# Kernel optimization log

Hardware: AMD Instinct MI355X
Metric: run time of the kernel (lower is better)

## Reference

```python
import jax, jax.numpy as jnp
import numpy as np

SAMPLING_FACTOR = 5


def setup_inputs() -> dict:
    key = jax.random.key(0)
    kq, kk, kv, ki = jax.random.split(key, 4)
    B, L, D = 32, 2048, 64
    return {
        "query_states": jax.random.normal(kq, (B, L, D), dtype=jnp.float32),
        "key_states": jax.random.normal(kk, (B, L, D), dtype=jnp.float32),
        "value_states": jax.random.normal(kv, (B, L, D), dtype=jnp.float32),
        "index_sample": jax.random.randint(ki, (L,), 0, L, dtype=jnp.int32),
    }


def reference(query_states, key_states, value_states, index_sample):
    B, L_Q, d_k = query_states.shape
    L_K = key_states.shape[1]
    log_L_K = int(np.ceil(np.log1p(L_K)))
    log_L_Q = int(np.ceil(np.log1p(L_Q)))
    U_part = min(SAMPLING_FACTOR * L_Q * log_L_K, L_K)
    u = min(SAMPLING_FACTOR * log_L_Q, L_Q)

    # random key sampling (indices supplied deterministically)
    idx = index_sample[:U_part]                       # [U_part]
    K_sample = jnp.take(key_states, idx, axis=1)      # [B, U_part, d]

    # sparsity measurement M(q) = max_k q.k - mean (original divides by L_K)
    Q_K_sample = jnp.einsum("bqd,bkd->bqk", query_states, K_sample)  # [B, L_Q, U_part]
    M = jnp.max(Q_K_sample, axis=-1) - jnp.sum(Q_K_sample, axis=-1) / jnp.float32(L_K)

    # top-u query selection
    _, M_top = jax.lax.top_k(M, u)                    # [B, u]
    Q_reduce = jnp.take_along_axis(query_states, M_top[..., None], axis=1)  # [B, u, d]

    # reduced attention
    attn_scores = jnp.einsum("bud,bkd->buk", Q_reduce, key_states) / jnp.sqrt(jnp.float32(d_k))
    attn_probs = jax.nn.softmax(attn_scores, axis=-1)
    attn_output = jnp.einsum("buk,bkd->bud", attn_probs, value_states)
    return attn_output, attn_scores
```

## Files before the change

### kernel.cpp

```cpp
#include <hip/hip_runtime.h>
#include <math.h>

#define BB 32
#define LL 2048
#define DD 64
#define UU 40
#define CC 64
#define FSEG 16
#define PSTR 42
#define NEG_BIG (-3.0e38f)

typedef __attribute__((ext_vector_type(8))) short short8;
typedef __attribute__((ext_vector_type(4))) float f32x4;
typedef unsigned long long ull;
typedef unsigned int uint;
typedef unsigned short ushort_t;

__device__ __forceinline__ unsigned short f2bf(float f) {
  uint u = __float_as_uint(f);
  u += 0x7FFFu + ((u >> 16) & 1u);
  return (unsigned short)(u >> 16);
}
__device__ __forceinline__ uint fsort(float f) {
  uint u = __float_as_uint(f);
  return (u & 0x80000000u) ? ~u : (u | 0x80000000u);
}
__device__ __forceinline__ ull shfl_xor_u64(ull x, int m) {
  uint lo = (uint)x, hi = (uint)(x >> 32);
  lo = __shfl_xor(lo, m);
  hi = __shfl_xor(hi, m);
  return ((ull)hi << 32) | lo;
}
__device__ __forceinline__ int4 pack_bf16x8(float4 a, float4 c4) {
  int4 o;
  o.x = (int)(f2bf(a.x) | ((uint)f2bf(a.y) << 16));
  o.y = (int)(f2bf(a.z) | ((uint)f2bf(a.w) << 16));
  o.z = (int)(f2bf(c4.x) | ((uint)f2bf(c4.y) << 16));
  o.w = (int)(f2bf(c4.z) | ((uint)f2bf(c4.w) << 16));
  return o;
}
__device__ __forceinline__ void async_copy16(const void* g, void* l) {
  __builtin_amdgcn_global_load_lds((const __attribute__((address_space(1))) void*)g,
                                   (__attribute__((address_space(3))) void*)l, 16, 0, 0);
}

__global__ __launch_bounds__(256) void prep_ksum_kernel(const float* __restrict__ K,
                                                        const int* __restrict__ idx,
                                                        ushort_t* __restrict__ Kg,
                                                        float* __restrict__ Kpart) {
  int p = blockIdx.x, b = blockIdx.y, t = threadIdx.x;
  int g = t & 7;
  float4 sa = {0.f, 0.f, 0.f, 0.f}, sb = {0.f, 0.f, 0.f, 0.f};
#pragma unroll
  for (int it = 0; it < 4; ++it) {
    int r = p * 128 + it * 32 + (t >> 3);
    int gk = idx[r];
    const float* src = K + ((size_t)b * LL + gk) * DD + g * 8;
    float4 a = *(const float4*)src;
    float4 c4 = *(const float4*)(src + 4);
    sa.x += a.x; sa.y += a.y; sa.z += a.z; sa.w += a.w;
    sb.x += c4.x; sb.y += c4.y; sb.z += c4.z; sb.w += c4.w;
    *(int4*)(Kg + ((size_t)b * LL + r) * DD + 8 * (g ^ (r & 7))) = pack_bf16x8(a, c4);
  }
  __shared__ float red[32][64];
  int rt = t >> 3;
  *(float4*)&red[rt][g * 8] = sa;
  *(float4*)&red[rt][g * 8 + 4] = sb;
  __syncthreads();
  if (t < 64) {
    float s = 0.f;
#pragma unroll
    for (int r = 0; r < 32; ++r) s += red[r][t];
    Kpart[(b * 16 + p) * 64 + t] = s;
  }
}

__global__ __launch_bounds__(256) void mfma_m_kernel(const float* __restrict__ Q,
                                                     const ushort_t* __restrict__ Kg,
                                                     const float* __restrict__ Kpart,
                                                     float* __restrict__ Mb) {
  __shared__ __align__(16) ushort_t Qs[128 * 64];
  __shared__ __align__(16) ushort_t Ks[2][128 * 64];
  __shared__ float Mmax[2][128];
  __shared__ float KsumS[64];

  int b = blockIdx.y, q0 = blockIdx.x * 128;
  int t = threadIdx.x;
  int w = t >> 6, L = t & 63;

  const ushort_t* KgB = Kg + (size_t)b * LL * DD;

#pragma unroll
  for (int i = 0; i < 4; ++i) {
    const ushort_t* gp =
        KgB + (size_t)(w * 32 + i * 8 + (L >> 3)) * DD + (L & 7) * 8;
    async_copy16(gp, &Ks[0][(w * 32 + i * 8) * 64]);
  }

  if (t < 64) {
    float s = 0.f;
#pragma unroll
    for (int p = 0; p < 16; ++p) s += Kpart[(b * 16 + p) * 64 + t];
    KsumS[t] = s;
  }

  {
    int g = t & 7;
#pragma unroll
    for (int it = 0; it < 4; ++it) {
      int r = it * 32 + (t >> 3);
      const float* src = Q + ((size_t)b * LL + q0 + r) * DD + g * 8;
      float4 a = *(const float4*)src;
      float4 c4 = *(const float4*)(src + 4);
      *(int4*)&Qs[r * 64 + 8 * (g ^ (r & 7))] = pack_bf16x8(a, c4);
    }
  }
  __syncthreads();

  f32x4 mx[4];
#pragma unroll
  for (int i = 0; i < 4; ++i) mx[i] = (f32x4){NEG_BIG, NEG_BIG, NEG_BIG, NEG_BIG};

  const int waveQ = 64 * (w & 1);
  const int waveK = 64 * (w >> 1);
  const int lm = L & 15;
  const int lq = L >> 4;

  for (int c = 0; c < LL / 128; ++c) {
    int cur = c & 1;
    if (c < LL / 128 - 1) {
      int nxt = cur ^ 1;
#pragma unroll
      for (int i = 0; i < 4; ++i) {
        const ushort_t* gp =
            KgB + (size_t)((c + 1) * 128 + w * 32 + i * 8 + (L >> 3)) * DD + (L & 7) * 8;
        async_copy16(gp, &Ks[nxt][(w * 32 + i * 8) * 64]);
      }
    }

    f32x4 acc[4][4];
#pragma unroll
    for (int i = 0; i < 4; ++i)
#pragma unroll
      for (int j = 0; j < 4; ++j) acc[i][j] = (f32x4){0.f, 0.f, 0.f, 0.f};

#pragma unroll
    for (int s = 0; s < 2; ++s) {
      int g = 4 * s + lq;
      short8 A[4];
#pragma unroll
      for (int qt = 0; qt < 4; ++qt) {
        int r = waveQ + 16 * qt + lm;
        A[qt] = *(const short8*)&Qs[r * 64 + 8 * (g ^ (r & 7))];
      }
#pragma unroll
      for (int kt = 0; kt < 4; ++kt) {
        int rB = waveK + 16 * kt + lm;
        short8 Bf = *(const short8*)&Ks[cur][rB * 64 + 8 * (g ^ (rB & 7))];
#pragma unroll
        for (int qt = 0; qt < 4; ++qt) {
          acc[qt][kt] = __builtin_amdgcn_mfma_f32_16x16x32_bf16(A[qt], Bf, acc[qt][kt], 0, 0, 0);
        }
      }
    }
#pragma unroll
    for (int qt = 0; qt < 4; ++qt)
#pragma unroll
      for (int kt = 0; kt < 4; ++kt) {
#pragma unroll
        for (int r4 = 0; r4 < 4; ++r4) mx[qt][r4] = fmaxf(mx[qt][r4], acc[qt][kt][r4]);
      }
    __syncthreads();
  }

#pragma unroll
  for (int qt = 0; qt < 4; ++qt) {
#pragma unroll
    for (int r4 = 0; r4 < 4; ++r4) {
      float v = mx[qt][r4];
      v = fmaxf(v, __shfl_xor(v, 1));
      v = fmaxf(v, __shfl_xor(v, 2));
      v = fmaxf(v, __shfl_xor(v, 4));
      v = fmaxf(v, __shfl_xor(v, 8));
      mx[qt][r4] = v;
    }
  }
  if (lm < 4) {
    int qt = lm;
#pragma unroll
    for (int r4 = 0; r4 < 4; ++r4) {
      Mmax[w >> 1][waveQ + 16 * qt + 4 * lq + r4] = mx[qt][r4];
    }
  }
  __syncthreads();

  if (t < 128) {
    float m = fmaxf(Mmax[0][t], Mmax[1][t]);
    const float4* Qr = (const float4*)(Q + ((size_t)b * LL + q0 + t) * DD);
    float s = 0.f;
#pragma unroll
    for (int i = 0; i < 16; ++i) {
      float4 qv = Qr[i];
      s += qv.x * KsumS[4 * i] + qv.y * KsumS[4 * i + 1] + qv.z * KsumS[4 * i + 2] +
           qv.w * KsumS[4 * i + 3];
    }
    Mb[b * LL + q0 + t] = m - s * (1.0f / (float)LL);
  }
}

__global__ __launch_bounds__(256) void cand_kernel(const float* __restrict__ Mb,
                                                   int* __restrict__ cand) {
  int b = blockIdx.x, t = threadIdx.x;
  int w = t >> 6;
  float v[8];
#pragma unroll
  for (int i = 0; i < 8; ++i) v[i] = Mb[b * LL + t + 256 * i];
  __shared__ ull warr[4];
  __shared__ ull winls;
  for (int round = 0; round < CC; ++round) {
    float bv = v[0];
    int bi = 0;
#pragma unroll
    for (int i = 1; i < 8; ++i)
      if (v[i] > bv) { bv = v[i]; bi = i; }
    ull key = ((ull)fsort(bv) << 32) | (ull)(uint)(t + 256 * bi);
#pragma unroll
    for (int m = 1; m < 64; m <<= 1) {
      ull o = shfl_xor_u64(key, m);
      if (o > key) key = o;
    }
    if ((t & 63) == 0) warr[w] = key;
    __syncthreads();
    if (t == 0) {
      ull k = warr[0];
#pragma unroll
      for (int i = 1; i < 4; ++i)
        if (warr[i] > k) k = warr[i];
      winls = k;
      cand[b * CC + round] = (int)(k & 0xFFFFFFFFull);
    }
    __syncthreads();
    int wj = (int)(winls & 0xFFFFFFFFull);
    if (t == (wj & 255)) v[wj >> 8] = NEG_BIG;
  }
}

__global__ __launch_bounds__(256) void rescue_kernel(const float* __restrict__ Q,
                                                     const float* __restrict__ K,
                                                     const int* __restrict__ idx,
                                                     const int* __restrict__ cand,
                                                     float* __restrict__ Mpart) {
  __shared__ float Qc[64][68];
  __shared__ float Kt[128][68];
  __shared__ float red[64][33];
  __shared__ int cidx[CC];
  int seg = blockIdx.x, b = blockIdx.y, t = threadIdx.x;

  if (t < CC) cidx[t] = cand[b * CC + t];
  __syncthreads();
  for (int li = t; li < 64 * 16; li += 256) {
    int row = li >> 4, g4 = li & 15;
    *(float4*)&Qc[row][4 * g4] =
        *(const float4*)(Q + ((size_t)b * LL + cidx[row]) * DD + 4 * g4);
  }
  for (int li = t; li < 128 * 16; li += 256) {
    int row = li >> 4, g4 = li & 15;
    int gk = idx[seg * 128 + row];
    *(float4*)&Kt[row][4 * g4] =
        *(const float4*)(K + ((size_t)b * LL + gk) * DD + 4 * g4);
  }
  __syncthreads();

  int tx = t & 7;
  int ty = t >> 3;
  float acc[8][4];
#pragma unroll
  for (int i = 0; i < 8; ++i)
#pragma unroll
    for (int j = 0; j < 4; ++j) acc[i][j] = 0.f;

#pragma unroll 4
  for (int dd = 0; dd < 64; dd += 4) {
    float4 qf[8];
#pragma unroll
    for (int i = 0; i < 8; ++i) qf[i] = *(const float4*)&Qc[tx + 8 * i][dd];
    float4 kf[4];
#pragma unroll
    for (int j = 0; j < 4; ++j) kf[j] = *(const float4*)&Kt[ty + 32 * j][dd];
#pragma unroll
    for (int i = 0; i < 8; ++i)
#pragma unroll
      for (int j = 0; j < 4; ++j) {
        float d = acc[i][j];
        d = fmaf(qf[i].x, kf[j].x, d);
        d = fmaf(qf[i].y, kf[j].y, d);
        d = fmaf(qf[i].z, kf[j].z, d);
        d = fmaf(qf[i].w, kf[j].w, d);
        acc[i][j] = d;
      }
  }

#pragma unroll
  for (int i = 0; i < 8; ++i) {
    float m = fmaxf(fmaxf(acc[i][0], acc[i][1]), fmaxf(acc[i][2], acc[i][3]));
    red[tx + 8 * i][ty] = m;
  }
  __syncthreads();
  if (t < CC) {
    float m = red[t][0];
#pragma unroll
    for (int tt = 1; tt < 32; ++tt) m = fmaxf(m, red[t][tt]);
    Mpart[((size_t)b * CC + t) * FSEG + seg] = m;
  }
}

__global__ __launch_bounds__(64) void select_kernel(const float* __restrict__ Q,
                                                    const float* __restrict__ Kpart,
                                                    const int* __restrict__ cand,
                                                    const float* __restrict__ Mpart,
                                                    int* __restrict__ topi) {
  int b = blockIdx.x, t = threadIdx.x;
  __shared__ float KsumS[64];
  __shared__ ull keys[CC];
  {
    float s = 0.f;
#pragma unroll
    for (int p = 0; p < 16; ++p) s += Kpart[(b * 16 + p) * 64 + t];
    KsumS[t] = s;
  }
  __syncthreads();
  int ci = cand[b * CC + t];
  float m = NEG_BIG;
#pragma unroll
  for (int s = 0; s < FSEG; ++s) m = fmaxf(m, Mpart[((size_t)b * CC + t) * FSEG + s]);
  const float4* Qr = (const float4*)(Q + ((size_t)b * LL + ci) * DD);
  float s = 0.f;
#pragma unroll
  for (int i = 0; i < 16; ++i) {
    float4 qv = Qr[i];
    s += qv.x * KsumS[4 * i] + qv.y * KsumS[4 * i + 1] + qv.z * KsumS[4 * i + 2] +
         qv.w * KsumS[4 * i + 3];
  }
  float Mf = m - s * (1.0f / (float)LL);
  ull key = ((ull)fsort(Mf) << 32) | (ull)(uint)(2047 - ci);
  keys[t] = key;
  __syncthreads();
  int rank = 0;
#pragma unroll 8
  for (int j = 0; j < CC; ++j) rank += (keys[j] > key) ? 1 : 0;
  if (rank < UU) topi[b * UU + rank] = ci;
}

__global__ __launch_bounds__(256, 2) void fused_epilogue_kernel(
    const float* __restrict__ Q, const float* __restrict__ K,
    const float* __restrict__ V, const int* __restrict__ topi,
    float* __restrict__ scores, float* __restrict__ Opart,
    float* __restrict__ lpart) {
  int seg = blockIdx.x, b = blockIdx.y, t = threadIdx.x;
  __shared__ int cidx[UU];
  __shared__ float Qc[UU][DD];
  __shared__ float pT[128 * PSTR];
  __shared__ float lw[4][20];

  if (t < UU) cidx[t] = topi[b * UU + t];
  __syncthreads();
  for (int li = t; li < UU * 16; li += 256) {
    int u = li >> 4, g4 = li & 15;
    *(float4*)&Qc[u][4 * g4] =
        *(const float4*)(Q + ((size_t)b * LL + cidx[u]) * DD + 4 * g4);
  }
  __syncthreads();

  int kl = t & 127, uh = t >> 7, w = t >> 6;
  int k = seg * 128 + kl;
  float4 kr[16];
  const float4* Krow = (const float4*)(K + ((size_t)b * LL + k) * DD);
#pragma unroll
  for (int i = 0; i < 16; ++i) kr[i] = Krow[i];

  float p[20];
#pragma unroll 4
  for (int j = 0; j < 20; ++j) {
    int u = uh * 20 + j;
    const float4* qp = (const float4*)&Qc[u][0];
    float s = 0.f;
#pragma unroll
    for (int i = 0; i < 16; ++i) {
      float4 qv = qp[i];
      s += qv.x * kr[i].x + qv.y * kr[i].y + qv.z * kr[i].z + qv.w * kr[i].w;
    }
    s *= 0.125f;
    scores[((size_t)(b * UU + u)) * LL + k] = s;
    p[j] = __expf(s);
  }

#pragma unroll
  for (int j = 0; j < 20; ++j) {
    float ls = p[j];
#pragma unroll
    for (int off = 32; off > 0; off >>= 1) ls += __shfl_xor(ls, off);
    if ((t & 63) == 0) lw[w][j] = ls;
  }
#pragma unroll
  for (int j = 0; j < 20; j += 2) {
    *(float2*)&pT[kl * PSTR + uh * 20 + j] = make_float2(p[j], p[j + 1]);
  }
  __syncthreads();
  if (t < UU) {
    int u = t;
    float ls = (u < 20) ? (lw[0][u] + lw[1][u]) : (lw[2][u - 20] + lw[3][u - 20]);
    lpart[(size_t)(b * FSEG + seg) * UU + u] = ls;
  }

  int d4 = t & 15, c = t >> 4;
  int ug = c & 7, kq = c >> 3;
  int u0 = ug * 5;
  float4 acc[5];
#pragma unroll
  for (int j = 0; j < 5; ++j) acc[j] = (float4){0.f, 0.f, 0.f, 0.f};
  const float* Vb = V + ((size_t)b * LL + seg * 128 + kq * 64) * DD;
  for (int kk = 0; kk < 64; ++kk) {
    float4 v4 = *(const float4*)(Vb + (size_t)kk * DD + 4 * d4);
    const float* prow = &pT[(kq * 64 + kk) * PSTR + u0];
#pragma unroll
    for (int j = 0; j < 5; ++j) {
      float pj = prow[j];
      acc[j].x += pj * v4.x; acc[j].y += pj * v4.y;
      acc[j].z += pj * v4.z; acc[j].w += pj * v4.w;
    }
  }
  __syncthreads();
  float* red = pT;
#pragma unroll
  for (int j = 0; j < 5; ++j)
    *(float4*)&red[(kq * 40 + u0 + j) * 64 + 4 * d4] = acc[j];
  __syncthreads();
  for (int li = t; li < UU * DD; li += 256) {
    int u = li >> 6, d = li & 63;
    float s = red[u * 64 + d] + red[(40 + u) * 64 + d];
    Opart[((size_t)(b * FSEG + seg) * UU + u) * DD + d] = s;
  }
}

__global__ __launch_bounds__(256) void combine_kernel(const float* __restrict__ Opart,
                                                      const float* __restrict__ lpart,
                                                      float* __restrict__ out) {
  int b = blockIdx.x, t = threadIdx.x;
  __shared__ float Linv[UU];
  if (t < UU) {
    float Lsum = 0.f;
#pragma unroll
    for (int s = 0; s < FSEG; ++s) Lsum += lpart[(size_t)(b * FSEG + s) * UU + t];
    Linv[t] = 1.0f / Lsum;
  }
  __syncthreads();
  for (int li = t; li < UU * DD; li += 256) {
    int u = li >> 6, d = li & 63;
    float O = 0.f;
#pragma unroll
    for (int s = 0; s < FSEG; ++s)
      O += Opart[((size_t)(b * FSEG + s) * UU + u) * DD + d];
    out[((size_t)b * UU + u) * DD + d] = O * Linv[u];
  }
}

__global__ __launch_bounds__(256) void ksum_kernel(const float* __restrict__ K,
                                                   const int* __restrict__ idx,
                                                   float* __restrict__ Kpart) {
  int p = blockIdx.x, b = blockIdx.y, tid = threadIdx.x;
  int d = tid & 63, c = tid >> 6;
  const float* Kb = K + (size_t)b * LL * DD;
  float acc = 0.f;
  int j0 = p * 128 + c * 32;
#pragma unroll 4
  for (int t = 0; t < 32; ++t) acc += Kb[(size_t)idx[j0 + t] * DD + d];
  __shared__ float red[256];
  red[tid] = acc;
  __syncthreads();
  if (c == 0) Kpart[(b * 16 + p) * 64 + d] = red[d] + red[64 + d] + red[128 + d] + red[192 + d];
}

__global__ __launch_bounds__(256) void m_kernel(const float* __restrict__ Q,
                                                const float* __restrict__ K,
                                                const int* __restrict__ idx,
                                                const float* __restrict__ Kpart,
                                                float* __restrict__ M) {
  __shared__ float Qs[128][68];
  __shared__ float Ks[128][68];
  __shared__ float KsumS[64];
  __shared__ float red[128][17];
  int b = blockIdx.y, q0 = blockIdx.x * 128, tid = threadIdx.x;
  int tx = tid & 15, ty = tid >> 4;
  if (tid < 64) {
    float s = 0.f;
#pragma unroll
    for (int p = 0; p < 16; ++p) s += Kpart[(b * 16 + p) * 64 + tid];
    KsumS[tid] = s;
  }
#pragma unroll
  for (int it = 0; it < 8; ++it) {
    int li = it * 256 + tid;
    int q = li >> 4, dd = (li & 15) << 2;
    *(float4*)&Qs[q][dd] = *(const float4*)(Q + ((size_t)b * LL + q0 + q) * DD + dd);
  }
  float mx[8];
#pragma unroll
  for (int i = 0; i < 8; ++i) mx[i] = NEG_BIG;
  for (int c = 0; c < LL / 128; ++c) {
    __syncthreads();
#pragma unroll
    for (int it = 0; it < 8; ++it) {
      int li = it * 256 + tid;
      int kk = li >> 4, dd = (li & 15) << 2;
      int gk = idx[c * 128 + kk];
      *(float4*)&Ks[kk][dd] = *(const float4*)(K + ((size_t)b * LL + gk) * DD + dd);
    }
    __syncthreads();
    float acc[8][8];
#pragma unroll
    for (int i = 0; i < 8; ++i)
#pragma unroll
      for (int j = 0; j < 8; ++j) acc[i][j] = 0.f;
#pragma unroll 2
    for (int dd = 0; dd < 64; dd += 4) {
      float4 qf[8];
#pragma unroll
      for (int i = 0; i < 8; ++i) qf[i] = *(const float4*)&Qs[tx + 16 * i][dd];
#pragma unroll
      for (int j = 0; j < 8; ++j) {
        float4 kf = *(const float4*)&Ks[ty + 16 * j][dd];
#pragma unroll
        for (int i = 0; i < 8; ++i)
          acc[i][j] += qf[i].x * kf.x + qf[i].y * kf.y + qf[i].z * kf.z + qf[i].w * kf.w;
      }
    }
#pragma unroll
    for (int i = 0; i < 8; ++i) {
      float m01 = fmaxf(fmaxf(acc[i][0], acc[i][1]), fmaxf(acc[i][2], acc[i][3]));
      float m23 = fmaxf(fmaxf(acc[i][4], acc[i][5]), fmaxf(acc[i][6], acc[i][7]));
      mx[i] = fmaxf(mx[i], fmaxf(m01, m23));
    }
  }
  __syncthreads();
#pragma unroll
  for (int i = 0; i < 8; ++i) red[tx + 16 * i][ty] = mx[i];
  __syncthreads();
  if (tid < 128) {
    float m = red[tid][0];
#pragma unroll
    for (int tt = 1; tt < 16; ++tt) m = fmaxf(m, red[tid][tt]);
    float s = 0.f;
#pragma unroll 16
    for (int d = 0; d < 64; ++d) s += Qs[tid][d] * KsumS[d];
    M[b * LL + q0 + tid] = m - s * (1.0f / (float)LL);
  }
}

__global__ __launch_bounds__(256) void topk_kernel(const float* __restrict__ M,
                                                   int* __restrict__ topi) {
  int b = blockIdx.x, tid = threadIdx.x;
  __shared__ float mv[LL];
  __shared__ float wv[4];
  __shared__ int wi[4];
  for (int j = tid; j < LL; j += 256) mv[j] = M[b * LL + j];
  __syncthreads();
  for (int t = 0; t < UU; ++t) {
    float bv = NEG_BIG;
    int bi = 0x7fffffff;
    for (int j = tid; j < LL; j += 256) {
      float v = mv[j];
      if (v > bv) { bv = v; bi = j; }
    }
#pragma unroll
    for (int off = 32; off > 0; off >>= 1) {
      float ov = __shfl_down(bv, off);
      int oi = __shfl_down(bi, off);
      if (ov > bv || (ov == bv && oi < bi)) { bv = ov; bi = oi; }
    }
    if ((tid & 63) == 0) { wv[tid >> 6] = bv; wi[tid >> 6] = bi; }
    __syncthreads();
    if (tid == 0) {
#pragma unroll
      for (int w = 1; w < 4; ++w)
        if (wv[w] > bv || (wv[w] == bv && wi[w] < bi)) { bv = wv[w]; bi = wi[w]; }
      topi[b * UU + t] = bi;
      mv[bi] = NEG_BIG;
    }
    __syncthreads();
  }
}

__global__ __launch_bounds__(256) void scores_kernel(const float* __restrict__ Q,
                                                     const float* __restrict__ K,
                                                     const int* __restrict__ topi,
                                                     float* __restrict__ scores) {
  int b = blockIdx.y;
  int k = blockIdx.x * 256 + threadIdx.x;
  __shared__ float Qr[UU][DD];
  for (int li = threadIdx.x; li < UU * DD; li += 256) {
    int u = li >> 6, d = li & 63;
    Qr[u][d] = Q[((size_t)b * LL + topi[b * UU + u]) * DD + d];
  }
  __syncthreads();
  float4 kr[16];
  const float4* Krow = (const float4*)(K + ((size_t)b * LL + k) * DD);
#pragma unroll
  for (int i = 0; i < 16; ++i) kr[i] = Krow[i];
  for (int u = 0; u < UU; ++u) {
    float s = 0.f;
#pragma unroll
    for (int i = 0; i < 16; ++i) {
      float4 qv = *(const float4*)&Qr[u][i << 2];
      s += qv.x * kr[i].x + qv.y * kr[i].y + qv.z * kr[i].z + qv.w * kr[i].w;
    }
    scores[((size_t)(b * UU + u)) * LL + k] = s * 0.125f;
  }
}

__global__ __launch_bounds__(256) void softmax_pv_kernel(const float* __restrict__ scores,
                                                         const float* __restrict__ V,
                                                         float* __restrict__ out) {
  int b = blockIdx.y;
  int u0 = blockIdx.x * 4;
  int tid = threadIdx.x;
  __shared__ float p[4][LL];
  __shared__ float wred[4];
  __shared__ float inv_s[4];
  __shared__ float r2[256];
#pragma unroll
  for (int uu = 0; uu < 4; ++uu) {
    const float* srow = scores + ((size_t)(b * UU + u0 + uu)) * LL;
    float m = NEG_BIG;
    for (int j = tid; j < LL; j += 256) m = fmaxf(m, srow[j]);
#pragma unroll
    for (int off = 32; off > 0; off >>= 1) m = fmaxf(m, __shfl_down(m, off));
    if ((tid & 63) == 0) wred[tid >> 6] = m;
    __syncthreads();
    float smax = fmaxf(fmaxf(wred[0], wred[1]), fmaxf(wred[2], wred[3]));
    __syncthreads();
    float ls = 0.f;
    for (int j = tid; j < LL; j += 256) {
      float e = __expf(srow[j] - smax);
      p[uu][j] = e;
      ls += e;
    }
#pragma unroll
    for (int off = 32; off > 0; off >>= 1) ls += __shfl_down(ls, off);
    if ((tid & 63) == 0) wred[tid >> 6] = ls;
    __syncthreads();
    if (tid == 0) inv_s[uu] = 1.0f / (wred[0] + wred[1] + wred[2] + wred[3]);
    __syncthreads();
  }
  int d = tid & 63, c = tid >> 6;
  float acc[4] = {0.f, 0.f, 0.f, 0.f};
  const float* Vb = V + (size_t)b * LL * DD;
  int k0 = c * (LL / 4), k1 = k0 + (LL / 4);
  for (int k = k0; k < k1; ++k) {
    float v = Vb[(size_t)k * DD + d];
#pragma unroll
    for (int uu = 0; uu < 4; ++uu) acc[uu] += p[uu][k] * v;
  }
#pragma unroll
  for (int uu = 0; uu < 4; ++uu) {
    r2[tid] = acc[uu];
    __syncthreads();
    if (c == 0) {
      out[((size_t)(b * UU) + u0 + uu) * DD + d] =
          (r2[d] + r2[64 + d] + r2[128 + d] + r2[192 + d]) * inv_s[uu];
    }
    __syncthreads();
  }
}

extern "C" void kernel_launch(void* const* d_in, const int* in_sizes, int n_in,
                              void* d_out, int out_size, void* d_ws, size_t ws_size,
                              hipStream_t stream) {
  (void)in_sizes; (void)n_in; (void)out_size;
  const float* Q = (const float*)d_in[0];
  const float* K = (const float*)d_in[1];
  const float* V = (const float*)d_in[2];
  const int* idx = (const int*)d_in[3];

  float* out = (float*)d_out;
  float* scores = out + (size_t)BB * UU * DD;

  const size_t kg_off = 0;
  const size_t kpart_off = kg_off + (size_t)BB * LL * DD * sizeof(ushort_t);
  const size_t mb_off = kpart_off + (size_t)BB * 16 * DD * sizeof(float);
  const size_t mpart_off = mb_off + (size_t)BB * LL * sizeof(float);
  const size_t cand_off = mpart_off + (size_t)BB * CC * FSEG * sizeof(float);
  const size_t topi_off = cand_off + (size_t)BB * CC * sizeof(int);
  const size_t need = topi_off + (size_t)BB * UU * sizeof(int);

  char* ws = (char*)d_ws;
  if (ws_size >= need) {
    ushort_t* Kg = (ushort_t*)(ws + kg_off);
    float* Kpart = (float*)(ws + kpart_off);
    float* Mb = (float*)(ws + mb_off);
    float* Mpart = (float*)(ws + mpart_off);
    int* cand = (int*)(ws + cand_off);
    int* topi = (int*)(ws + topi_off);
    float* Opart = (float*)(ws + kg_off);
    float* lpart = Opart + (size_t)BB * FSEG * UU * DD;

    prep_ksum_kernel<<<dim3(16, BB), 256, 0, stream>>>(K, idx, Kg, Kpart);
    mfma_m_kernel<<<dim3(LL / 128, BB), 256, 0, stream>>>(Q, Kg, Kpart, Mb);
    cand_kernel<<<BB, 256, 0, stream>>>(Mb, cand);
    rescue_kernel<<<dim3(FSEG, BB), 256, 0, stream>>>(Q, K, idx, cand, Mpart);
    select_kernel<<<BB, 64, 0, stream>>>(Q, Kpart, cand, Mpart, topi);
    fused_epilogue_kernel<<<dim3(FSEG, BB), 256, 0, stream>>>(Q, K, V, topi, scores,
                                                              Opart, lpart);
    combine_kernel<<<BB, 256, 0, stream>>>(Opart, lpart, out);
  } else {
    size_t need2 =
        (size_t)(BB * LL + BB * 16 * DD) * sizeof(float) + (size_t)(BB * UU) * sizeof(int);
    float* M;
    float* Kpart;
    int* topi;
    if (ws_size >= need2) {
      M = (float*)d_ws;
      Kpart = M + BB * LL;
      topi = (int*)(Kpart + BB * 16 * DD);
    } else {
      M = scores;
      Kpart = scores + BB * LL;
      topi = (int*)out;
    }
    ksum_kernel<<<dim3(16, BB), 256, 0, stream>>>(K, idx, Kpart);
    m_kernel<<<dim3(LL / 128, BB), 256, 0, stream>>>(Q, K, idx, Kpart, M);
    topk_kernel<<<BB, 256, 0, stream>>>(M, topi);
    scores_kernel<<<dim3(LL / 256, BB), 256, 0, stream>>>(Q, K, topi, scores);
    softmax_pv_kernel<<<dim3(UU / 4, BB), 256, 0, stream>>>(scores, V, out);
  }
}
```

Measured before the change: 203.9 us.

## Split epilogue blocks by query half and register-tile QK scores

The fused epilogue grid doubles so that each block handles 20 of the 40 selected queries for a 128-key segment. Within a block, each thread now computes 5 queries against 2 keys instead of 20 queries against 1 key, which cuts the register-held K row and reuses each LDS Q load across two keys. The PV reduction is re-split into 4 key quarters with a padded reduction stride. The grid gets more parallelism and lower register pressure, at the cost of reading each K and V segment twice from global memory.

```diff
diff --git a/kernel.cpp b/kernel.cpp
--- a/kernel.cpp
+++ b/kernel.cpp
@@ -7,7 +7,8 @@
 #define UU 40
 #define CC 64
 #define FSEG 16
-#define PSTR 42
+#define PSTR2 21
+#define RSTR 68
 #define NEG_BIG (-3.0e38f)
 
 typedef __attribute__((ext_vector_type(8))) short short8;
@@ -356,72 +357,79 @@
     const float* __restrict__ V, const int* __restrict__ topi,
     float* __restrict__ scores, float* __restrict__ Opart,
     float* __restrict__ lpart) {
-  int seg = blockIdx.x, b = blockIdx.y, t = threadIdx.x;
-  __shared__ int cidx[UU];
-  __shared__ float Qc[UU][DD];
-  __shared__ float pT[128 * PSTR];
-  __shared__ float lw[4][20];
-
-  if (t < UU) cidx[t] = topi[b * UU + t];
-  __syncthreads();
-  for (int li = t; li < UU * 16; li += 256) {
+  int bx = blockIdx.x;
+  int seg = bx >> 1, uh2 = bx & 1;
+  int b = blockIdx.y, t = threadIdx.x;
+  __shared__ int cidx[20];
+  __shared__ float Qc[20][DD];
+  __shared__ float pTred[4 * 20 * RSTR];
+
+  if (t < 20) cidx[t] = topi[b * UU + uh2 * 20 + t];
+  __syncthreads();
+  for (int li = t; li < 20 * 16; li += 256) {
     int u = li >> 4, g4 = li & 15;
     *(float4*)&Qc[u][4 * g4] =
         *(const float4*)(Q + ((size_t)b * LL + cidx[u]) * DD + 4 * g4);
   }
   __syncthreads();
 
-  int kl = t & 127, uh = t >> 7, w = t >> 6;
-  int k = seg * 128 + kl;
-  float4 kr[16];
-  const float4* Krow = (const float4*)(K + ((size_t)b * LL + k) * DD);
-#pragma unroll
-  for (int i = 0; i < 16; ++i) kr[i] = Krow[i];
-
-  float p[20];
-#pragma unroll 4
-  for (int j = 0; j < 20; ++j) {
-    int u = uh * 20 + j;
-    const float4* qp = (const float4*)&Qc[u][0];
-    float s = 0.f;
-#pragma unroll
-    for (int i = 0; i < 16; ++i) {
-      float4 qv = qp[i];
-      s += qv.x * kr[i].x + qv.y * kr[i].y + qv.z * kr[i].z + qv.w * kr[i].w;
-    }
-    s *= 0.125f;
-    scores[((size_t)(b * UU + u)) * LL + k] = s;
-    p[j] = __expf(s);
-  }
-
-#pragma unroll
-  for (int j = 0; j < 20; ++j) {
-    float ls = p[j];
+  float* pT = pTred;
+
+  int kp = t & 63, ug = t >> 6;
+  int u0 = ug * 5;
+  int k0 = seg * 128 + kp;
+  const float4* K0 = (const float4*)(K + ((size_t)b * LL + k0) * DD);
+  const float4* K1 = (const float4*)(K + ((size_t)b * LL + k0 + 64) * DD);
+  float s0[5] = {0.f, 0.f, 0.f, 0.f, 0.f};
+  float s1[5] = {0.f, 0.f, 0.f, 0.f, 0.f};
+#pragma unroll
+  for (int i = 0; i < 16; ++i) {
+    float4 ka = K0[i];
+    float4 kb = K1[i];
+#pragma unroll
+    for (int j = 0; j < 5; ++j) {
+      float4 qv = *(const float4*)&Qc[u0 + j][4 * i];
+      s0[j] += qv.x * ka.x + qv.y * ka.y + qv.z * ka.z + qv.w * ka.w;
+      s1[j] += qv.x * kb.x + qv.y * kb.y + qv.z * kb.z + qv.w * kb.w;
+    }
+  }
+
+  float p0[5], p1[5];
+#pragma unroll
+  for (int j = 0; j < 5; ++j) {
+    float sa = s0[j] * 0.125f, sb = s1[j] * 0.125f;
+    int u = uh2 * 20 + u0 + j;
+    scores[((size_t)(b * UU + u)) * LL + k0] = sa;
+    scores[((size_t)(b * UU + u)) * LL + k0 + 64] = sb;
+    p0[j] = __expf(sa);
+    p1[j] = __expf(sb);
+  }
+
+#pragma unroll
+  for (int j = 0; j < 5; ++j) {
+    float ls = p0[j] + p1[j];
 #pragma unroll
     for (int off = 32; off > 0; off >>= 1) ls += __shfl_xor(ls, off);
-    if ((t & 63) == 0) lw[w][j] = ls;
-  }
-#pragma unroll
-  for (int j = 0; j < 20; j += 2) {
-    *(float2*)&pT[kl * PSTR + uh * 20 + j] = make_float2(p[j], p[j + 1]);
-  }
-  __syncthreads();
-  if (t < UU) {
-    int u = t;
-    float ls = (u < 20) ? (lw[0][u] + lw[1][u]) : (lw[2][u - 20] + lw[3][u - 20]);
-    lpart[(size_t)(b * FSEG + seg) * UU + u] = ls;
-  }
+    if (kp == 0)
+      lpart[(size_t)(b * FSEG + seg) * UU + uh2 * 20 + u0 + j] = ls;
+  }
+#pragma unroll
+  for (int j = 0; j < 5; ++j) {
+    pT[kp * PSTR2 + u0 + j] = p0[j];
+    pT[(kp + 64) * PSTR2 + u0 + j] = p1[j];
+  }
+  __syncthreads();
 
   int d4 = t & 15, c = t >> 4;
-  int ug = c & 7, kq = c >> 3;
-  int u0 = ug * 5;
+  int ug3 = c & 3, kq = c >> 2;
+  int uu0 = ug3 * 5;
   float4 acc[5];
 #pragma unroll
   for (int j = 0; j < 5; ++j) acc[j] = (float4){0.f, 0.f, 0.f, 0.f};
-  const float* Vb = V + ((size_t)b * LL + seg * 128 + kq * 64) * DD;
-  for (int kk = 0; kk < 64; ++kk) {
+  const float* Vb = V + ((size_t)b * LL + seg * 128 + kq * 32) * DD;
+  for (int kk = 0; kk < 32; ++kk) {
     float4 v4 = *(const float4*)(Vb + (size_t)kk * DD + 4 * d4);
-    const float* prow = &pT[(kq * 64 + kk) * PSTR + u0];
+    const float* prow = &pT[(kq * 32 + kk) * PSTR2 + uu0];
 #pragma unroll
     for (int j = 0; j < 5; ++j) {
       float pj = prow[j];
@@ -430,15 +438,16 @@
     }
   }
   __syncthreads();
-  float* red = pT;
+  float* red = pTred;
 #pragma unroll
   for (int j = 0; j < 5; ++j)
-    *(float4*)&red[(kq * 40 + u0 + j) * 64 + 4 * d4] = acc[j];
-  __syncthreads();
-  for (int li = t; li < UU * DD; li += 256) {
+    *(float4*)&red[(kq * 20 + uu0 + j) * RSTR + 4 * d4] = acc[j];
+  __syncthreads();
+  for (int li = t; li < 20 * DD; li += 256) {
     int u = li >> 6, d = li & 63;
-    float s = red[u * 64 + d] + red[(40 + u) * 64 + d];
-    Opart[((size_t)(b * FSEG + seg) * UU + u) * DD + d] = s;
+    float s = red[(0 * 20 + u) * RSTR + d] + red[(1 * 20 + u) * RSTR + d] +
+              red[(2 * 20 + u) * RSTR + d] + red[(3 * 20 + u) * RSTR + d];
+    Opart[((size_t)(b * FSEG + seg) * UU + uh2 * 20 + u) * DD + d] = s;
   }
 }
 
@@ -708,8 +717,8 @@
     cand_kernel<<<BB, 256, 0, stream>>>(Mb, cand);
     rescue_kernel<<<dim3(FSEG, BB), 256, 0, stream>>>(Q, K, idx, cand, Mpart);
     select_kernel<<<BB, 64, 0, stream>>>(Q, Kpart, cand, Mpart, topi);
-    fused_epilogue_kernel<<<dim3(FSEG, BB), 256, 0, stream>>>(Q, K, V, topi, scores,
-                                                              Opart, lpart);
+    fused_epilogue_kernel<<<dim3(FSEG * 2, BB), 256, 0, stream>>>(Q, K, V, topi, scores,
+                                                                  Opart, lpart);
     combine_kernel<<<BB, 256, 0, stream>>>(Opart, lpart, out);
   } else {
     size_t need2 =
```

Result: no change. 201.8 us (-1.0%).
